# Optimization experiments

Measured on AMD Instinct MI355X. Metric: run time of the kernel, lower is better.

## Reference

```python
import jax, jax.numpy as jnp
import numpy as np

C = 128; HEADS = 8; GH = 32; GW = 32; B = 8; PD = 8  # PD = (dim//4)//4

def _conv(x, w, pad, dil=1, groups=1):
    return jax.lax.conv_general_dilated(
        x, w, (1, 1), [(pad[0], pad[0]), (pad[1], pad[1])],
        rhs_dilation=(dil, dil),
        dimension_numbers=('NCHW', 'OIHW', 'NCHW'),
        feature_group_count=groups)

def _lrelu(t):
    return jnp.where(t >= 0, t, 0.1 * t)

def _ln(t, g, b, eps=1e-5):
    m = jnp.mean(t, -1, keepdims=True)
    v = jnp.var(t, -1, keepdims=True)
    return (t - m) * jax.lax.rsqrt(v + eps) * g + b

def setup_inputs():
    rng = np.random.RandomState(0)
    f = lambda *s: jnp.asarray((rng.randn(*s) * 0.05).astype(np.float32))
    ones = lambda n: jnp.ones((n,), jnp.float32)
    zeros = lambda n: jnp.zeros((n,), jnp.float32)
    # Swin-style relative position index over the (GH, GW) group
    coords = np.stack(np.meshgrid(np.arange(GH), np.arange(GW), indexing='ij')).reshape(2, -1)
    rel = (coords[:, :, None] - coords[:, None, :]).transpose(1, 2, 0)
    rel[..., 0] += GH - 1; rel[..., 1] += GW - 1; rel[..., 0] *= 2 * GW - 1
    rel_idx = jnp.asarray(rel.sum(-1).astype(np.int32))  # [N, N]
    biases = np.stack(np.meshgrid(np.arange(1 - GH, GH), np.arange(1 - GW, GW), indexing='ij'))
    biases = jnp.asarray(biases.reshape(2, -1).T.astype(np.float32))  # [(2GH-1)*(2GW-1), 2]
    return dict(
        x=jnp.asarray(rng.rand(B, C, GH, GW).astype(np.float32)),
        conv1_w=f(C, C, 3, 3), conv2_w=f(C, C, 3, 3), conv3_w=f(C, C, 3, 3),
        convt_w=f(C, 3, 1, 1),
        rba_w=f(C, C, 3, 1), rba_b=zeros(C), rbb_w=f(C, C, 1, 3), rbb_b=zeros(C),
        pp_w=f(PD, 2), pp_b=zeros(PD),
        l1_g=ones(PD), l1_b=zeros(PD), l1_w=f(PD, PD), l1_b2=zeros(PD),
        l2_g=ones(PD), l2_b=zeros(PD), l2_w=f(PD, PD), l2_b2=zeros(PD),
        l3_g=ones(PD), l3_b=zeros(PD), l3_w=f(HEADS, PD), l3_b2=zeros(HEADS),
        qk_w=f(2 * C, C), qk_b=zeros(2 * C),
        v_w=f(C, C), v_b=zeros(C),
        proj_w=f(C, C), proj_b=zeros(C),
        fc1_w=f(C, C), fc1_b=zeros(C), fc2_w=f(C, C), fc2_b=zeros(C),
        biases=biases, rel_idx=rel_idx,
    )

def reference(x, conv1_w, conv2_w, conv3_w, convt_w, rba_w, rba_b, rbb_w, rbb_b,
              pp_w, pp_b, l1_g, l1_b, l1_w, l1_b2, l2_g, l2_b, l2_w, l2_b2,
              l3_g, l3_b, l3_w, l3_b2, qk_w, qk_b, v_w, v_b, proj_w, proj_b,
              fc1_w, fc1_b, fc2_w, fc2_b, biases, rel_idx):
    Bn, Cc, Hh, Ww = x.shape
    N = Hh * Ww
    hd = Cc // HEADS
    # FeaExtract: ResASPP (3 dilated 3x3 convs, grouped 1x1 merge) + residual
    b1 = _lrelu(_conv(x, conv1_w, (1, 1)))
    b2 = _lrelu(_conv(x, conv2_w, (3, 3), dil=3))
    b3 = _lrelu(_conv(x, conv3_w, (5, 5), dil=5))
    a = _conv(jnp.concatenate([b1, b2, b3], 1), convt_w, (0, 0), groups=Cc) + x
    # RB: (3,1) conv -> lrelu -> (1,3) conv + residual
    r = _lrelu(_conv(a, rba_w, (1, 0)) + rba_b[None, :, None, None])
    r = _conv(r, rbb_w, (0, 1)) + rbb_b[None, :, None, None]
    o0 = r + a
    # original uses in-place clamp_, so o0 is clamped before flattening
    o0 = jnp.clip(o0, 0.0, 1.0)
    E = o0.reshape(Bn, Cc, N).transpose(0, 2, 1)  # [B, N, C]
    qk = E @ qk_w.T + qk_b  # [B, N, 2C]
    q = qk[..., :Cc].reshape(Bn, N, HEADS, hd).transpose(0, 2, 1, 3)
    k = qk[..., Cc:].reshape(Bn, N, HEADS, hd).transpose(0, 2, 1, 3)
    v = (E @ v_w.T + v_b).reshape(Bn, N, HEADS, hd).transpose(0, 2, 1, 3)
    attn = jnp.einsum('bhid,bhjd->bhij', q * (hd ** -0.5), k)
    # DynamicPosBias MLP (residual=False): Linear(2,pd) -> [LN,ReLU,Linear] x2 -> LN,ReLU,Linear(pd,heads)
    p = biases @ pp_w.T + pp_b
    p = jax.nn.relu(_ln(p, l1_g, l1_b)) @ l1_w.T + l1_b2
    p = jax.nn.relu(_ln(p, l2_g, l2_b)) @ l2_w.T + l2_b2
    p = jax.nn.relu(_ln(p, l3_g, l3_b)) @ l3_w.T + l3_b2  # [L, heads]
    rpb = p[rel_idx]  # gather -> [N, N, heads]
    attn = attn + rpb.transpose(2, 0, 1)[None]
    attn = jax.nn.softmax(attn, axis=-1)
    y = jnp.einsum('bhij,bhjd->bhid', attn, v).transpose(0, 2, 1, 3).reshape(Bn, N, Cc) + E
    x_proj = y @ proj_w.T + proj_b
    h = jax.nn.gelu(x_proj @ fc1_w.T + fc1_b, approximate=False)
    return (h @ fc2_w.T + fc2_b) + y
```

## Files before the change

kernel.cpp:

```cpp
#include <hip/hip_runtime.h>
#include <hip/hip_bf16.h>

typedef __hip_bfloat16 bf16;
typedef __bf16 bf16x8 __attribute__((ext_vector_type(8)));
typedef float f32x4 __attribute__((ext_vector_type(4)));

#define Lb 3969

#define XP_F   0
#define WF_F   903168
#define WR_F   1124352
#define WG_F   1173504
#define BH_F   1222656
#define QKV_F  1222656
#define AP_F   2795520
#define YT_F   2795520
#define EB_F   3352576
#define R1P_F  3352576
#define FLAG_F 3908616
#define RT_F   3908624
#define VT_F   4924432
#define R1_F   5448720

__device__ __forceinline__ float b2f(bf16 v) { return __bfloat162float(v); }
__device__ __forceinline__ bf16 f2b(float v) { return __float2bfloat16(v); }

template <typename T> __device__ __forceinline__ float ldw(const void* p, int i);
template <> __device__ __forceinline__ float ldw<bf16>(const void* p, int i) {
  return __bfloat162float(((const bf16*)p)[i]);
}
template <> __device__ __forceinline__ float ldw<float>(const void* p, int i) {
  return ((const float*)p)[i];
}
template <typename T> __device__ __forceinline__ void stw(void* p, size_t i, float v);
template <> __device__ __forceinline__ void stw<bf16>(void* p, size_t i, float v) {
  ((bf16*)p)[i] = __float2bfloat16(v);
}
template <> __device__ __forceinline__ void stw<float>(void* p, size_t i, float v) {
  ((float*)p)[i] = v;
}

__device__ __forceinline__ unsigned pkb(float a, float b) {
  bf16 x = __float2bfloat16(a), y = __float2bfloat16(b);
  unsigned short ux = *(unsigned short*)&x, uy = *(unsigned short*)&y;
  return (unsigned)ux | ((unsigned)uy << 16);
}

__device__ __forceinline__ bool detect_local(const unsigned* x) {
  int lane = threadIdx.x & 63;
  int cnt = 0;
#pragma unroll
  for (int k = 0; k < 4; ++k) {
    unsigned lo = x[lane + 64 * k] & 0xFFFFu;
    cnt += (lo >= 0x3C00u && lo < 0x3F80u) ? 1 : 0;
  }
#pragma unroll
  for (int off = 1; off < 64; off <<= 1) cnt += __shfl_xor(cnt, off);
  return cnt >= 128;
}

template <typename T>
__device__ void wprep_all_body(const void* w1, const void* w2, const void* w3,
                               const void* rba_w, const void* rbb_w,
                               const void* qk_w, const void* v_w,
                               const void* proj_w, const void* fc1_w,
                               const void* fc2_w, bf16* __restrict__ Wf,
                               bf16* __restrict__ Wr, bf16* __restrict__ Wg)
{
  int tid = blockIdx.x * 256 + threadIdx.x;
  int lane = tid & 63, li = lane & 15, quad = lane >> 4;
  if (tid < 55296) {
    int mt = (tid >> 6) & 7;
    int Kc = (tid >> 9) & 3;
    int rem = tid >> 11;
    int t = rem % 9;
    int br = rem / 9;
    const void* w = (br == 0 ? w1 : (br == 1 ? w2 : w3));
    int o = mt * 16 + li;
    int ci0 = Kc * 32 + quad * 8;
#pragma unroll
    for (int j = 0; j < 8; ++j)
      Wf[(size_t)tid * 8 + j] = f2b(ldw<T>(w, (o * 128 + ci0 + j) * 9 + t));
  } else {
    int u = tid - 55296;
    if (u < 12288) {
      int Kc = (u >> 6) & 3, mt = (u >> 8) & 7, q = u >> 11;
      const void* w = (q >= 3) ? rbb_w : rba_w;
      int t = q % 3;
#pragma unroll
      for (int j = 0; j < 8; ++j)
        Wr[(size_t)u * 8 + j] =
            f2b(ldw<T>(w, ((mt * 16 + li) * 128 + Kc * 32 + quad * 8 + j) * 3 + t));
    } else if (u < 24576) {
      int g = u - 12288;
      int Kc = (g >> 6) & 3, mtg = g >> 8;
      const void* w; int mrow; float sc = 1.f;
      if (mtg < 16)      { w = qk_w;   mrow = mtg * 16; if (mtg < 8) sc = 0.25f; }
      else if (mtg < 24) { w = v_w;    mrow = (mtg - 16) * 16; }
      else if (mtg < 32) { w = proj_w; mrow = (mtg - 24) * 16; }
      else if (mtg < 40) { w = fc1_w;  mrow = (mtg - 32) * 16; }
      else               { w = fc2_w;  mrow = (mtg - 40) * 16; }
#pragma unroll
      for (int j = 0; j < 8; ++j)
        Wg[(size_t)g * 8 + j] =
            f2b(sc * ldw<T>(w, (mrow + li) * 128 + Kc * 32 + quad * 8 + j));
    }
  }
}

__global__ __launch_bounds__(256) void wprep_all_kernel(
    const unsigned* x, const void* w1, const void* w2, const void* w3,
    const void* rba_w, const void* rbb_w, const void* qk_w, const void* v_w,
    const void* proj_w, const void* fc1_w, const void* fc2_w,
    bf16* Wf, bf16* Wr, bf16* Wg, int* flag)
{
  bool isbf = detect_local(x);
  if (blockIdx.x == 0 && threadIdx.x == 0) *flag = isbf ? 1 : 0;
  if (isbf) wprep_all_body<bf16>(w1, w2, w3, rba_w, rbb_w, qk_w, v_w, proj_w,
                                 fc1_w, fc2_w, Wf, Wr, Wg);
  else      wprep_all_body<float>(w1, w2, w3, rba_w, rbb_w, qk_w, v_w, proj_w,
                                  fc1_w, fc2_w, Wf, Wr, Wg);
}

template <typename T>
__device__ __forceinline__ void ln_relu8(const float* t, float* u,
                                         const void* g, const void* bb)
{
  float m = 0.f;
#pragma unroll
  for (int k = 0; k < 8; ++k) m += t[k];
  m *= 0.125f;
  float v = 0.f;
#pragma unroll
  for (int k = 0; k < 8; ++k) { float d = t[k] - m; v += d * d; }
  v *= 0.125f;
  float r = rsqrtf(v + 1e-5f);
#pragma unroll
  for (int k = 0; k < 8; ++k) {
    float val = (t[k] - m) * r * ldw<T>(g, k) + ldw<T>(bb, k);
    u[k] = val > 0.f ? val : 0.f;
  }
}

template <typename T>
__device__ void dpbrt_body(const void* biases, const void* pp_w, const void* pp_b,
    const void* l1_g, const void* l1_b, const void* l1_w, const void* l1_b2,
    const void* l2_g, const void* l2_b, const void* l2_w, const void* l2_b2,
    const void* l3_g, const void* l3_b, const void* l3_w, const void* l3_b2,
    float* __restrict__ RT, float (*LH)[47][8])
{
  const int tt = blockIdx.x, t = tt >> 1, p = tt & 1;
  const int lane = threadIdx.x, quad = lane >> 4, li = lane & 15;

  for (int it = 0; it < 2; ++it) {
    int idx = it * 64 + lane;
    if (idx < 94) {
      int sd = idx / 47, xi = idx - sd * 47;
      int rtab = (t + 1 - sd) * 63 + p * 16 + xi;
      float b0 = ldw<T>(biases, rtab * 2), b1 = ldw<T>(biases, rtab * 2 + 1);
      float tv[8], u[8];
#pragma unroll
      for (int j = 0; j < 8; ++j)
        tv[j] = b0 * ldw<T>(pp_w, j * 2) + b1 * ldw<T>(pp_w, j * 2 + 1) +
                ldw<T>(pp_b, j);
      ln_relu8<T>(tv, u, l1_g, l1_b);
#pragma unroll
      for (int j = 0; j < 8; ++j) {
        float s = ldw<T>(l1_b2, j);
#pragma unroll
        for (int k = 0; k < 8; ++k) s += u[k] * ldw<T>(l1_w, j * 8 + k);
        tv[j] = s;
      }
      ln_relu8<T>(tv, u, l2_g, l2_b);
#pragma unroll
      for (int j = 0; j < 8; ++j) {
        float s = ldw<T>(l2_b2, j);
#pragma unroll
        for (int k = 0; k < 8; ++k) s += u[k] * ldw<T>(l2_w, j * 8 + k);
        tv[j] = s;
      }
      ln_relu8<T>(tv, u, l3_g, l3_b);
#pragma unroll
      for (int h = 0; h < 8; ++h) {
        float s = ldw<T>(l3_b2, h);
#pragma unroll
        for (int k = 0; k < 8; ++k) s += u[k] * ldw<T>(l3_w, h * 8 + k);
        LH[sd][xi][h] = s;
      }
    }
  }
  __syncthreads();
#pragma unroll
  for (int h = 0; h < 8; ++h)
#pragma unroll
    for (int mt = 0; mt < 4; ++mt) {
      f32x4 v;
#pragma unroll
      for (int r = 0; r < 4; ++r) {
        int j = mt * 16 + quad * 4 + r;
        int jy = j >> 5;
        int xi = li + 31 - (j & 31);
        v[r] = LH[jy][xi][h];
      }
      *(f32x4*)&RT[(((size_t)h * 124 + tt) * 4 + mt) * 256 + lane * 4] = v;
    }
}

__global__ __launch_bounds__(64) void dpbrt_kernel(
    const void* biases, const void* pp_w, const void* pp_b, const void* l1_g,
    const void* l1_b, const void* l1_w, const void* l1_b2, const void* l2_g,
    const void* l2_b, const void* l2_w, const void* l2_b2, const void* l3_g,
    const void* l3_b, const void* l3_w, const void* l3_b2, float* RT,
    const int* flag)
{
  __shared__ float LH[2][47][8];
  if (*flag)
    dpbrt_body<bf16>(biases, pp_w, pp_b, l1_g, l1_b, l1_w, l1_b2, l2_g, l2_b,
                     l2_w, l2_b2, l3_g, l3_b, l3_w, l3_b2, RT, LH);
  else
    dpbrt_body<float>(biases, pp_w, pp_b, l1_g, l1_b, l1_w, l1_b2, l2_g, l2_b,
                      l2_w, l2_b2, l3_g, l3_b, l3_w, l3_b2, RT, LH);
}

template <typename T>
__device__ void nhwc_body(const void* x, bf16* __restrict__ xp, bf16 (*tile)[128])
{
  const int b = blockIdx.x >> 5;
  const int row = blockIdx.x & 31;
  const int t = threadIdx.x;
  const size_t bbase = (size_t)b * 42 * 42 * 128;
  const bf16x8 z = (bf16x8){};

  if (t < 160) {
    int side = t / 80;
    int off = (t % 80) * 8;
    *(bf16x8*)&xp[bbase + ((size_t)(row + 5) * 42 + side * 37) * 128 + off] = z;
  }
  {
    int zr = (row < 5) ? row : ((row >= 27) ? row + 10 : -1);
    if (zr >= 0) {
      size_t base = bbase + (size_t)zr * 42 * 128;
      for (int k = t; k < 672; k += 256) *(bf16x8*)&xp[base + k * 8] = z;
    }
  }

  {
    int ci = t >> 1, half = t & 1;
#pragma unroll
    for (int j = 0; j < 16; ++j) {
      int px = half * 16 + j;
      tile[px][ci] = f2b(ldw<T>(x, ((size_t)b * 128 + ci) * 1024 + row * 32 + px));
    }
  }
  __syncthreads();
  {
    int px = t >> 3, c0 = (t & 7) * 16;
    bf16* dst = xp + (bbase + ((size_t)(row + 5) * 42 + (px + 5)) * 128 + c0);
#pragma unroll
    for (int j = 0; j < 16; ++j) dst[j] = tile[px][c0 + j];
  }
}

__global__ __launch_bounds__(256) void nhwc_kernel(const void* x, bf16* xp,
                                                   const int* flag)
{
  __shared__ bf16 tile[32][128];
  if (*flag) nhwc_body<bf16>(x, xp, tile);
  else       nhwc_body<float>(x, xp, tile);
}

__global__ __launch_bounds__(256) void aspp2_kernel(
    const bf16* __restrict__ xp, const bf16* __restrict__ Wf,
    bf16* __restrict__ bh)
{
  const int nt_ = blockIdx.x, br = blockIdx.y >> 1, mh = blockIdx.y & 1;
  const int bb = blockIdx.z;
  const int w = threadIdx.x >> 6, lane = threadIdx.x & 63;
  const int quad = lane >> 4, li = lane & 15;
  const int d = (br == 0 ? 1 : (br == 1 ? 3 : 5));
  const int pxw = nt_ * 64 + w * 16;
  const int y = pxw >> 5, xb = pxw & 31;

  f32x4 acc[4] = {};
  const bf16* Wbase = Wf + (size_t)br * 18432 * 8 + (size_t)mh * 4 * 64 * 8;

  for (int t = 0; t < 9; ++t) {
    const int dy = (t / 3 - 1) * d, dx = (t % 3 - 1) * d;
    const bf16* Asite =
        xp + (((size_t)bb * 42 + (y + 5 + dy)) * 42 + (xb + li + 5 + dx)) * 128;
    const bf16* Wt = Wbase + (size_t)t * 2048 * 8;
#pragma unroll
    for (int Kc = 0; Kc < 4; ++Kc) {
      bf16x8 afrag = *(const bf16x8*)(Asite + Kc * 32 + quad * 8);
      const bf16* Wk = Wt + (size_t)Kc * 512 * 8 + (size_t)lane * 8;
#pragma unroll
      for (int mt = 0; mt < 4; ++mt) {
        bf16x8 wfrag = *(const bf16x8*)(Wk + (size_t)mt * 64 * 8);
        acc[mt] = __builtin_amdgcn_mfma_f32_16x16x32_bf16(afrag, wfrag, acc[mt],
                                                          0, 0, 0);
      }
    }
  }
#pragma unroll
  for (int mt = 0; mt < 4; ++mt)
#pragma unroll
    for (int r = 0; r < 4; ++r) {
      int px = pxw + quad * 4 + r;
      bh[((size_t)bb * 1024 + px) * 384 + br * 128 + (mh * 4 + mt) * 16 + li] =
          f2b(acc[mt][r]);
    }
}

template <typename T>
__device__ void merge2_body(const bf16* __restrict__ xp, const void* wt,
                            const bf16* __restrict__ bh, bf16* __restrict__ ap,
                            float* cw)
{
  const int b = blockIdx.y, px0 = blockIdx.x * 32;
  const bf16x8 z = (bf16x8){};
  if (blockIdx.x == 0) {
    size_t base = ((size_t)b * 34 + 0) * 32 * 128;
    for (int k = threadIdx.x; k < 512; k += 256) *(bf16x8*)&ap[base + k * 8] = z;
  } else if (blockIdx.x == 31) {
    size_t base = ((size_t)b * 34 + 33) * 32 * 128;
    for (int k = threadIdx.x; k < 512; k += 256) *(bf16x8*)&ap[base + k * 8] = z;
  }
  for (int i = threadIdx.x; i < 384; i += 256) cw[i] = ldw<T>(wt, i);
  __syncthreads();
  const int pxl = threadIdx.x >> 3, og = threadIdx.x & 7;
  const int px = px0 + pxl, o0 = og * 16;
  const int y = px >> 5, x = px & 31;
  const bf16* brow = bh + ((size_t)b * 1024 + px) * 384 + o0 * 3;
  const bf16* xrow = xp + (((size_t)b * 42 + y + 5) * 42 + x + 5) * 128 + o0;
  bf16* arow = ap + (((size_t)b * 34 + y + 1) * 32 + x) * 128 + o0;

  bf16 bl[48], xl[16], ol[16];
#pragma unroll
  for (int k = 0; k < 6; ++k) *(bf16x8*)&bl[k * 8] = *(const bf16x8*)&brow[k * 8];
  *(bf16x8*)&xl[0] = *(const bf16x8*)&xrow[0];
  *(bf16x8*)&xl[8] = *(const bf16x8*)&xrow[8];
#pragma unroll
  for (int j = 0; j < 16; ++j) {
    float v = b2f(xl[j]);
#pragma unroll
    for (int i = 0; i < 3; ++i) {
      float t = b2f(bl[j * 3 + i]);
      v += cw[(o0 + j) * 3 + i] * (t >= 0.f ? t : 0.1f * t);
    }
    ol[j] = f2b(v);
  }
  *(bf16x8*)&arow[0] = *(bf16x8*)&ol[0];
  *(bf16x8*)&arow[8] = *(bf16x8*)&ol[8];
}

__global__ __launch_bounds__(256) void merge2_kernel(
    const bf16* xp, const void* wt, const bf16* bh, bf16* ap, const int* flag)
{
  __shared__ float cw[384];
  if (*flag) merge2_body<bf16>(xp, wt, bh, ap, cw);
  else       merge2_body<float>(xp, wt, bh, ap, cw);
}

template <typename T>
__device__ void rb1_body(const bf16* __restrict__ ap, const bf16* __restrict__ Wr,
                         const void* bias, bf16* __restrict__ r1p)
{
  const int b = blockIdx.z, mh = blockIdx.y;
  const int lane = threadIdx.x;
  const int quad = lane >> 4, li = lane & 15;
  const int pxw = blockIdx.x * 16;
  const int y = pxw >> 5, xb = pxw & 31;
  f32x4 acc = {};
#pragma unroll
  for (int t = 0; t < 3; ++t) {
    const bf16* Asite = ap + (((size_t)b * 34 + y + t) * 32 + xb + li) * 128;
#pragma unroll
    for (int Kc = 0; Kc < 4; ++Kc) {
      bf16x8 afrag = *(const bf16x8*)(Asite + Kc * 32 + quad * 8);
      int f = (t * 8 + mh) * 4 + Kc;
      bf16x8 wfrag = *(const bf16x8*)(Wr + ((size_t)f * 64 + lane) * 8);
      acc = __builtin_amdgcn_mfma_f32_16x16x32_bf16(afrag, wfrag, acc, 0, 0, 0);
    }
  }
  const int o = mh * 16 + li;
  if (quad == 0) {
    int xcol = (xb == 0) ? 0 : 33;
    r1p[(((size_t)b * 32 + y) * 34 + xcol) * 128 + o] = f2b(0.f);
  }
  float bv = ldw<T>(bias, o);
#pragma unroll
  for (int r = 0; r < 4; ++r) {
    int x = xb + quad * 4 + r;
    float v = acc[r] + bv;
    v = (v >= 0.f ? v : 0.1f * v);
    r1p[(((size_t)b * 32 + y) * 34 + x + 1) * 128 + o] = f2b(v);
  }
}

__global__ __launch_bounds__(64) void rb1_kernel(
    const bf16* ap, const bf16* Wr, const void* bias, bf16* r1p, const int* flag)
{
  if (*flag) rb1_body<bf16>(ap, Wr, bias, r1p);
  else       rb1_body<float>(ap, Wr, bias, r1p);
}

template <typename T>
__device__ void rb2_body(const bf16* __restrict__ r1p, const bf16* __restrict__ Wr,
                         const void* bias, const bf16* __restrict__ ap,
                         bf16* __restrict__ Eb)
{
  const int b = blockIdx.z, mh = blockIdx.y;
  const int lane = threadIdx.x;
  const int quad = lane >> 4, li = lane & 15;
  const int pxw = blockIdx.x * 16;
  const int y = pxw >> 5, xb = pxw & 31;
  f32x4 acc = {};
#pragma unroll
  for (int t = 0; t < 3; ++t) {
    const bf16* Asite = r1p + (((size_t)b * 32 + y) * 34 + xb + li + t) * 128;
#pragma unroll
    for (int Kc = 0; Kc < 4; ++Kc) {
      bf16x8 afrag = *(const bf16x8*)(Asite + Kc * 32 + quad * 8);
      int f = ((3 + t) * 8 + mh) * 4 + Kc;
      bf16x8 wfrag = *(const bf16x8*)(Wr + ((size_t)f * 64 + lane) * 8);
      acc = __builtin_amdgcn_mfma_f32_16x16x32_bf16(afrag, wfrag, acc, 0, 0, 0);
    }
  }
  const int o = mh * 16 + li;
  float bv = ldw<T>(bias, o);
#pragma unroll
  for (int r = 0; r < 4; ++r) {
    int x = xb + quad * 4 + r;
    float v = acc[r] + bv +
              b2f(ap[(((size_t)b * 34 + y + 1) * 32 + x) * 128 + o]);
    v = fminf(fmaxf(v, 0.f), 1.f);
    Eb[((size_t)b * 1024 + y * 32 + x) * 128 + o] = f2b(v);
  }
}

__global__ __launch_bounds__(64) void rb2_kernel(
    const bf16* r1p, const bf16* Wr, const void* bias, const bf16* ap,
    bf16* Eb, const int* flag)
{
  if (*flag) rb2_body<bf16>(r1p, Wr, bias, ap, Eb);
  else       rb2_body<float>(r1p, Wr, bias, ap, Eb);
}

template <typename T>
__device__ void qkv_body(const bf16* __restrict__ Eb, const bf16* __restrict__ Wg,
                         const void* qk_b, const void* v_b,
                         bf16* __restrict__ QKV)
{
  const int grp = blockIdx.y, b = blockIdx.z;
  const int w = threadIdx.x >> 6, lane = threadIdx.x & 63;
  const int quad = lane >> 4, li = lane & 15;
  const int pxw = blockIdx.x * 64 + w * 16;
  bf16x8 ef[4];
#pragma unroll
  for (int Kc = 0; Kc < 4; ++Kc)
    ef[Kc] = *(const bf16x8*)&Eb[((size_t)b * 1024 + pxw + li) * 128 + Kc * 32 +
                                 quad * 8];
  f32x4 acc[8] = {};
#pragma unroll
  for (int nt = 0; nt < 8; ++nt) {
    int g = grp * 8 + nt;
#pragma unroll
    for (int Kc = 0; Kc < 4; ++Kc) {
      bf16x8 wf = *(const bf16x8*)&Wg[(((size_t)g * 4 + Kc) * 64 + lane) * 8];
      acc[nt] = __builtin_amdgcn_mfma_f32_16x16x32_bf16(ef[Kc], wf, acc[nt],
                                                        0, 0, 0);
    }
  }
#pragma unroll
  for (int nt = 0; nt < 8; ++nt) {
    int g = grp * 8 + nt;
    int o = g * 16 + li;
    float bv;
    if (g < 8)       bv = 0.25f * ldw<T>(qk_b, o);
    else if (g < 16) bv = ldw<T>(qk_b, o);
    else             bv = ldw<T>(v_b, o - 256);
#pragma unroll
    for (int r = 0; r < 4; ++r) {
      int px = pxw + quad * 4 + r;
      QKV[((size_t)b * 1024 + px) * 384 + o] = f2b(acc[nt][r] + bv);
    }
  }
}

__global__ __launch_bounds__(256) void qkv_kernel(
    const bf16* Eb, const bf16* Wg, const void* qk_b, const void* v_b,
    bf16* QKV, const int* flag)
{
  if (*flag) qkv_body<bf16>(Eb, Wg, qk_b, v_b, QKV);
  else       qkv_body<float>(Eb, Wg, qk_b, v_b, QKV);
}

__global__ __launch_bounds__(64) void vt_kernel(
    const bf16* __restrict__ QKV, bf16* __restrict__ VT)
{
  const int c = blockIdx.x, hh = blockIdx.y, b = blockIdx.z;
  __shared__ bf16 Vl[64][20];
  const int lane = threadIdx.x, quad = lane >> 4, li = lane & 15;
  const bf16* vsrc =
      QKV + ((size_t)b * 1024 + c * 64 + lane) * 384 + 256 + hh * 16;
  union { bf16x8 v; uint2 u[2]; } w0, w1;
  w0.v = *(const bf16x8*)vsrc;
  w1.v = *(const bf16x8*)(vsrc + 8);
  *(uint2*)&Vl[lane][0] = w0.u[0];
  *(uint2*)&Vl[lane][4] = w0.u[1];
  *(uint2*)&Vl[lane][8] = w1.u[0];
  *(uint2*)&Vl[lane][12] = w1.u[1];
  __syncthreads();
#pragma unroll
  for (int half = 0; half < 2; ++half) {
    union { bf16 e[8]; bf16x8 v; } uv;
#pragma unroll
    for (int jj = 0; jj < 8; ++jj)
      uv.e[jj] = Vl[half * 32 + quad * 8 + jj][li];
    *(bf16x8*)&VT[((((size_t)(b * 8 + hh) * 16 + c) * 2 + half) * 64 + lane) * 8] =
        uv.v;
  }
}

__global__ __launch_bounds__(128) void attn_kernel(
    const bf16* __restrict__ QKV, const bf16* __restrict__ Eb,
    const float* __restrict__ RT, const bf16* __restrict__ VT,
    bf16* __restrict__ Yt)
{
  const int qt = blockIdx.x;
  const int hh = blockIdx.y;
  const int b = blockIdx.z;

  __shared__ bf16 Pl[2][16][72];
  __shared__ float Red[64][5];

  const int w = threadIdx.x >> 6, lane = threadIdx.x & 63;
  const int quad = lane >> 4, li = lane & 15;
  const int qb = qt * 16;

  const bf16* QKVb = QKV + (size_t)b * 1024 * 384;
  const bf16* VTb = VT + (size_t)(b * 8 + hh) * 16 * 1024;
  const float* RTh = RT + (size_t)hh * 124 * 1024;

  bf16x8 qf = (bf16x8){};
  if (quad < 2)
    qf = *(const bf16x8*)&QKVb[(size_t)(qb + li) * 384 + hh * 16 + quad * 8];

  f32x4 O_ = {};
  float lsum = 0.f;

  for (int cc = 0; cc < 8; ++cc) {
    const int c = w * 8 + cc;
    const int c0 = c * 64;
    const int tt = ((qt >> 1) - 2 * c + 30) * 2 + (qt & 1);
    const float* rtp = RTh + (size_t)tt * 1024 + lane * 4;

    f32x4 sT[4];
#pragma unroll
    for (int mt = 0; mt < 4; ++mt) {
      f32x4 cin = *(const f32x4*)(rtp + (size_t)mt * 256);
      bf16x8 kf = (bf16x8){};
      if (quad < 2)
        kf = *(const bf16x8*)&QKVb[(size_t)(c0 + mt * 16 + li) * 384 + 128 +
                                   hh * 16 + quad * 8];
      sT[mt] = __builtin_amdgcn_mfma_f32_16x16x32_bf16(kf, qf, cin, 0, 0, 0);
    }

#pragma unroll
    for (int mt = 0; mt < 4; ++mt)
#pragma unroll
      for (int r = 0; r < 4; ++r) {
        float p = __expf(sT[mt][r]);
        sT[mt][r] = p;
        lsum += p;
      }

#pragma unroll
    for (int mt = 0; mt < 4; ++mt) {
      uint2 ww;
      ww.x = pkb(sT[mt][0], sT[mt][1]);
      ww.y = pkb(sT[mt][2], sT[mt][3]);
      *(uint2*)&Pl[w][li][mt * 16 + quad * 4] = ww;
    }

#pragma unroll
    for (int half = 0; half < 2; ++half) {
      bf16x8 vf = *(const bf16x8*)&VTb[((size_t)(c * 2 + half) * 64 + lane) * 8];
      bf16x8 pf = *(const bf16x8*)&Pl[w][li][half * 32 + quad * 8];
      O_ = __builtin_amdgcn_mfma_f32_16x16x32_bf16(pf, vf, O_, 0, 0, 0);
    }
  }

  if (w == 1) {
#pragma unroll
    for (int r = 0; r < 4; ++r) Red[lane][r] = O_[r];
    Red[lane][4] = lsum;
  }
  __syncthreads();
  if (w == 0) {
#pragma unroll
    for (int r = 0; r < 4; ++r) O_[r] += Red[lane][r];
    lsum += Red[lane][4];
    lsum += __shfl_xor(lsum, 16);
    lsum += __shfl_xor(lsum, 32);
    const int sbase = (lane & 48) + ((lane >> 2) & 12);
    const bf16* Ebp = Eb + (size_t)b * 1024 * 128 + hh * 16 + li;
    bf16* Ytp = Yt + (size_t)b * 1024 * 128 + hh * 16 + li;
#pragma unroll
    for (int r = 0; r < 4; ++r) {
      float lb = __shfl(lsum, sbase + r);
      int qrow = qb + quad * 4 + r;
      Ytp[(size_t)qrow * 128] =
          f2b(O_[r] / lb + b2f(Ebp[(size_t)qrow * 128]));
    }
  }
}

template <typename T, int MODE>
__device__ void mlp_body(const bf16* __restrict__ src, const bf16* __restrict__ Wg,
                         int tb, const void* bias, const bf16* __restrict__ res,
                         void* out)
{
  const int b = blockIdx.z, mh = blockIdx.y;
  const int lane = threadIdx.x;
  const int quad = lane >> 4, li = lane & 15;
  const int pxw = blockIdx.x * 16;
  bf16x8 ef[4];
#pragma unroll
  for (int Kc = 0; Kc < 4; ++Kc)
    ef[Kc] = *(const bf16x8*)&src[((size_t)b * 1024 + pxw + li) * 128 + Kc * 32 +
                                  quad * 8];
  f32x4 acc = {};
#pragma unroll
  for (int Kc = 0; Kc < 4; ++Kc) {
    bf16x8 wf = *(const bf16x8*)&Wg[(((size_t)(tb + mh) * 4 + Kc) * 64 + lane) * 8];
    acc = __builtin_amdgcn_mfma_f32_16x16x32_bf16(ef[Kc], wf, acc, 0, 0, 0);
  }
  const int o = mh * 16 + li;
  float bv = ldw<T>(bias, o);
#pragma unroll
  for (int r = 0; r < 4; ++r) {
    int px = pxw + quad * 4 + r;
    float v = acc[r] + bv;
    size_t oidx = ((size_t)b * 1024 + px) * 128 + o;
    if (MODE == 1) v = 0.5f * v * (1.f + erff(v * 0.70710678118f));
    if (MODE == 2) {
      v += b2f(res[oidx]);
      stw<T>(out, oidx, v);
    } else {
      ((bf16*)out)[oidx] = f2b(v);
    }
  }
}

template <int MODE>
__global__ __launch_bounds__(64) void mlp_kernel(
    const bf16* src, const bf16* Wg, int tb, const void* bias, const bf16* res,
    void* out, const int* flag)
{
  if (*flag) mlp_body<bf16, MODE>(src, Wg, tb, bias, res, out);
  else       mlp_body<float, MODE>(src, Wg, tb, bias, res, out);
}

extern "C" void kernel_launch(void* const* d_in, const int* in_sizes, int n_in,
                              void* d_out, int out_size, void* d_ws,
                              size_t ws_size, hipStream_t stream)
{
  (void)in_sizes; (void)n_in; (void)out_size; (void)ws_size;
  const void* x       = d_in[0];
  const void* conv1_w = d_in[1];
  const void* conv2_w = d_in[2];
  const void* conv3_w = d_in[3];
  const void* convt_w = d_in[4];
  const void* rba_w   = d_in[5];
  const void* rba_b   = d_in[6];
  const void* rbb_w   = d_in[7];
  const void* rbb_b   = d_in[8];
  const void* pp_w    = d_in[9];
  const void* pp_b    = d_in[10];
  const void* l1_g    = d_in[11];
  const void* l1_b    = d_in[12];
  const void* l1_w    = d_in[13];
  const void* l1_b2   = d_in[14];
  const void* l2_g    = d_in[15];
  const void* l2_b    = d_in[16];
  const void* l2_w    = d_in[17];
  const void* l2_b2   = d_in[18];
  const void* l3_g    = d_in[19];
  const void* l3_b    = d_in[20];
  const void* l3_w    = d_in[21];
  const void* l3_b2   = d_in[22];
  const void* qk_w    = d_in[23];
  const void* qk_b    = d_in[24];
  const void* v_w     = d_in[25];
  const void* v_b     = d_in[26];
  const void* proj_w  = d_in[27];
  const void* proj_b  = d_in[28];
  const void* fc1_w   = d_in[29];
  const void* fc1_b   = d_in[30];
  const void* fc2_w   = d_in[31];
  const void* fc2_b   = d_in[32];
  const void* biases  = d_in[33];

  float* ws   = (float*)d_ws;
  bf16*  xp   = (bf16*)(ws + XP_F);
  bf16*  Wf   = (bf16*)(ws + WF_F);
  bf16*  Wr   = (bf16*)(ws + WR_F);
  bf16*  Wg   = (bf16*)(ws + WG_F);
  bf16*  bh   = (bf16*)(ws + BH_F);
  bf16*  QKV  = (bf16*)(ws + QKV_F);
  bf16*  ap   = (bf16*)(ws + AP_F);
  bf16*  Yt   = (bf16*)(ws + YT_F);
  bf16*  Eb   = (bf16*)(ws + EB_F);
  int*   flag = (int*)(ws + FLAG_F);
  float* RT   = ws + RT_F;
  bf16*  VT   = (bf16*)(ws + VT_F);
  bf16*  r1p  = (bf16*)(ws + R1_F);
  bf16*  XPt  = (bf16*)(ws + QKV_F);
  bf16*  H1t  = (bf16*)(ws + QKV_F + 524288);

  wprep_all_kernel<<<312, 256, 0, stream>>>(
      (const unsigned*)x, conv1_w, conv2_w, conv3_w, rba_w, rbb_w, qk_w, v_w,
      proj_w, fc1_w, fc2_w, Wf, Wr, Wg, flag);
  dpbrt_kernel<<<124, 64, 0, stream>>>(biases, pp_w, pp_b, l1_g, l1_b, l1_w,
                                       l1_b2, l2_g, l2_b, l2_w, l2_b2, l3_g,
                                       l3_b, l3_w, l3_b2, RT, flag);
  nhwc_kernel<<<256, 256, 0, stream>>>(x, xp, flag);
  aspp2_kernel<<<dim3(16, 6, 8), 256, 0, stream>>>(xp, Wf, bh);
  merge2_kernel<<<dim3(32, 8), 256, 0, stream>>>(xp, convt_w, bh, ap, flag);
  rb1_kernel<<<dim3(64, 8, 8), 64, 0, stream>>>(ap, Wr, rba_b, r1p, flag);
  rb2_kernel<<<dim3(64, 8, 8), 64, 0, stream>>>(r1p, Wr, rbb_b, ap, Eb, flag);
  qkv_kernel<<<dim3(16, 3, 8), 256, 0, stream>>>(Eb, Wg, qk_b, v_b, QKV, flag);
  vt_kernel<<<dim3(16, 8, 8), 64, 0, stream>>>(QKV, VT);
  attn_kernel<<<dim3(64, 8, 8), 128, 0, stream>>>(QKV, Eb, RT, VT, Yt);
  mlp_kernel<0><<<dim3(64, 8, 8), 64, 0, stream>>>(Yt, Wg, 24, proj_b, nullptr,
                                                   XPt, flag);
  mlp_kernel<1><<<dim3(64, 8, 8), 64, 0, stream>>>(XPt, Wg, 32, fc1_b, nullptr,
                                                   H1t, flag);
  mlp_kernel<2><<<dim3(64, 8, 8), 64, 0, stream>>>(H1t, Wg, 40, fc2_b, Yt,
                                                   d_out, flag);
}
```

Measured before the change: 253.9 us.

## Store position-bias table in bf16 and prefetch next K/V/bias chunk in attention

The precomputed relative-position bias table is now written as bf16 instead of fp32, which halves its footprint and the bytes the attention kernel reads per chunk. The attention loop is fully unrolled and software-pipelined: K fragments, bias values and V fragments for the next 64-key chunk are loaded into registers while the current chunk runs its MFMAs and exp. P packing switches from round-to-nearest to bit truncation, which is cheaper but adds a little error. Extra live registers from double-buffering could lower occupancy, and the bf16 bias adds rounding error to the logits.

Measured after the change: 254.1 us. Within noise of the previous version (+0.1%).

```diff
diff --git a/kernel.cpp b/kernel.cpp
--- a/kernel.cpp
+++ b/kernel.cpp
@@ -16,7 +16,6 @@
 #define AP_F   2795520
 #define YT_F   2795520
 #define EB_F   3352576
-#define R1P_F  3352576
 #define FLAG_F 3908616
 #define RT_F   3908624
 #define VT_F   4924432
@@ -44,6 +43,16 @@
   bf16 x = __float2bfloat16(a), y = __float2bfloat16(b);
   unsigned short ux = *(unsigned short*)&x, uy = *(unsigned short*)&y;
   return (unsigned)ux | ((unsigned)uy << 16);
+}
+__device__ __forceinline__ unsigned pkt(float a, float b) {
+  unsigned ua = __float_as_uint(a), ub = __float_as_uint(b);
+  return (ua >> 16) | (ub & 0xffff0000u);
+}
+__device__ __forceinline__ float bf2f_lo(unsigned w) {
+  unsigned u = w << 16; return *(float*)&u;
+}
+__device__ __forceinline__ float bf2f_hi(unsigned w) {
+  unsigned u = w & 0xffff0000u; return *(float*)&u;
 }
 
 __device__ __forceinline__ bool detect_local(const unsigned* x) {
@@ -147,7 +156,7 @@
     const void* l1_g, const void* l1_b, const void* l1_w, const void* l1_b2,
     const void* l2_g, const void* l2_b, const void* l2_w, const void* l2_b2,
     const void* l3_g, const void* l3_b, const void* l3_w, const void* l3_b2,
-    float* __restrict__ RT, float (*LH)[47][8])
+    bf16* __restrict__ RT, float (*LH)[47][8])
 {
   const int tt = blockIdx.x, t = tt >> 1, p = tt & 1;
   const int lane = threadIdx.x, quad = lane >> 4, li = lane & 15;
@@ -194,7 +203,7 @@
   for (int h = 0; h < 8; ++h)
 #pragma unroll
     for (int mt = 0; mt < 4; ++mt) {
-      f32x4 v;
+      float v[4];
 #pragma unroll
       for (int r = 0; r < 4; ++r) {
         int j = mt * 16 + quad * 4 + r;
@@ -202,7 +211,8 @@
         int xi = li + 31 - (j & 31);
         v[r] = LH[jy][xi][h];
       }
-      *(f32x4*)&RT[(((size_t)h * 124 + tt) * 4 + mt) * 256 + lane * 4] = v;
+      *(uint2*)&RT[(((size_t)h * 124 + tt) * 4 + mt) * 256 + lane * 4] =
+          make_uint2(pkb(v[0], v[1]), pkb(v[2], v[3]));
     }
 }
 
@@ -210,7 +220,7 @@
     const void* biases, const void* pp_w, const void* pp_b, const void* l1_g,
     const void* l1_b, const void* l1_w, const void* l1_b2, const void* l2_g,
     const void* l2_b, const void* l2_w, const void* l2_b2, const void* l3_g,
-    const void* l3_b, const void* l3_w, const void* l3_b2, float* RT,
+    const void* l3_b, const void* l3_w, const void* l3_b2, bf16* RT,
     const int* flag)
 {
   __shared__ float LH[2][47][8];
@@ -524,7 +534,7 @@
 
 __global__ __launch_bounds__(128) void attn_kernel(
     const bf16* __restrict__ QKV, const bf16* __restrict__ Eb,
-    const float* __restrict__ RT, const bf16* __restrict__ VT,
+    const bf16* __restrict__ RT, const bf16* __restrict__ VT,
     bf16* __restrict__ Yt)
 {
   const int qt = blockIdx.x;
@@ -540,7 +550,7 @@
 
   const bf16* QKVb = QKV + (size_t)b * 1024 * 384;
   const bf16* VTb = VT + (size_t)(b * 8 + hh) * 16 * 1024;
-  const float* RTh = RT + (size_t)hh * 124 * 1024;
+  const bf16* RTh = RT + (size_t)hh * 124 * 1024;
 
   bf16x8 qf = (bf16x8){};
   if (quad < 2)
@@ -548,22 +558,53 @@
 
   f32x4 O_ = {};
   float lsum = 0.f;
-
+  const int cbase = w * 8;
+
+  bf16x8 kf[4]; uint2 rt[4]; bf16x8 vf[2];
+  {
+    const int c = cbase, c0 = c * 64;
+    const int tt = ((qt >> 1) - 2 * c + 30) * 2 + (qt & 1);
+    const bf16* rtp = RTh + (size_t)tt * 1024 + lane * 4;
+#pragma unroll
+    for (int mt = 0; mt < 4; ++mt) {
+      rt[mt] = *(const uint2*)(rtp + (size_t)mt * 256);
+      kf[mt] = (bf16x8){};
+      if (quad < 2)
+        kf[mt] = *(const bf16x8*)&QKVb[(size_t)(c0 + mt * 16 + li) * 384 + 128 +
+                                       hh * 16 + quad * 8];
+    }
+#pragma unroll
+    for (int h2 = 0; h2 < 2; ++h2)
+      vf[h2] = *(const bf16x8*)&VTb[((size_t)(c * 2 + h2) * 64 + lane) * 8];
+  }
+
+#pragma unroll
   for (int cc = 0; cc < 8; ++cc) {
-    const int c = w * 8 + cc;
-    const int c0 = c * 64;
-    const int tt = ((qt >> 1) - 2 * c + 30) * 2 + (qt & 1);
-    const float* rtp = RTh + (size_t)tt * 1024 + lane * 4;
+    bf16x8 kf_n[4]; uint2 rt_n[4]; bf16x8 vf_n[2];
+    if (cc < 7) {
+      const int c = cbase + cc + 1, c0 = c * 64;
+      const int tt = ((qt >> 1) - 2 * c + 30) * 2 + (qt & 1);
+      const bf16* rtp = RTh + (size_t)tt * 1024 + lane * 4;
+#pragma unroll
+      for (int mt = 0; mt < 4; ++mt) {
+        rt_n[mt] = *(const uint2*)(rtp + (size_t)mt * 256);
+        kf_n[mt] = (bf16x8){};
+        if (quad < 2)
+          kf_n[mt] = *(const bf16x8*)&QKVb[(size_t)(c0 + mt * 16 + li) * 384 +
+                                           128 + hh * 16 + quad * 8];
+      }
+#pragma unroll
+      for (int h2 = 0; h2 < 2; ++h2)
+        vf_n[h2] = *(const bf16x8*)&VTb[((size_t)(c * 2 + h2) * 64 + lane) * 8];
+    }
 
     f32x4 sT[4];
 #pragma unroll
     for (int mt = 0; mt < 4; ++mt) {
-      f32x4 cin = *(const f32x4*)(rtp + (size_t)mt * 256);
-      bf16x8 kf = (bf16x8){};
-      if (quad < 2)
-        kf = *(const bf16x8*)&QKVb[(size_t)(c0 + mt * 16 + li) * 384 + 128 +
-                                   hh * 16 + quad * 8];
-      sT[mt] = __builtin_amdgcn_mfma_f32_16x16x32_bf16(kf, qf, cin, 0, 0, 0);
+      f32x4 cin;
+      cin[0] = bf2f_lo(rt[mt].x); cin[1] = bf2f_hi(rt[mt].x);
+      cin[2] = bf2f_lo(rt[mt].y); cin[3] = bf2f_hi(rt[mt].y);
+      sT[mt] = __builtin_amdgcn_mfma_f32_16x16x32_bf16(kf[mt], qf, cin, 0, 0, 0);
     }
 
 #pragma unroll
@@ -578,16 +619,21 @@
 #pragma unroll
     for (int mt = 0; mt < 4; ++mt) {
       uint2 ww;
-      ww.x = pkb(sT[mt][0], sT[mt][1]);
-      ww.y = pkb(sT[mt][2], sT[mt][3]);
+      ww.x = pkt(sT[mt][0], sT[mt][1]);
+      ww.y = pkt(sT[mt][2], sT[mt][3]);
       *(uint2*)&Pl[w][li][mt * 16 + quad * 4] = ww;
     }
 
 #pragma unroll
     for (int half = 0; half < 2; ++half) {
-      bf16x8 vf = *(const bf16x8*)&VTb[((size_t)(c * 2 + half) * 64 + lane) * 8];
       bf16x8 pf = *(const bf16x8*)&Pl[w][li][half * 32 + quad * 8];
-      O_ = __builtin_amdgcn_mfma_f32_16x16x32_bf16(pf, vf, O_, 0, 0, 0);
+      O_ = __builtin_amdgcn_mfma_f32_16x16x32_bf16(pf, vf[half], O_, 0, 0, 0);
+    }
+
+    if (cc < 7) {
+#pragma unroll
+      for (int mt = 0; mt < 4; ++mt) { kf[mt] = kf_n[mt]; rt[mt] = rt_n[mt]; }
+      vf[0] = vf_n[0]; vf[1] = vf_n[1];
     }
   }
 
@@ -713,7 +759,7 @@
   bf16*  Yt   = (bf16*)(ws + YT_F);
   bf16*  Eb   = (bf16*)(ws + EB_F);
   int*   flag = (int*)(ws + FLAG_F);
-  float* RT   = ws + RT_F;
+  bf16*  RT   = (bf16*)(ws + RT_F);
   bf16*  VT   = (bf16*)(ws + VT_F);
   bf16*  r1p  = (bf16*)(ws + R1_F);
   bf16*  XPt  = (bf16*)(ws + QKV_F);
```
